# Kernel optimization log

Measured on AMD Instinct MI355X. Metric: run time of the kernel, lower is better.

Reference implementation:

```python
import jax, jax.numpy as jnp
import numpy as np

NUM_HEADS = 16
HEAD_DIM = 64  # embedding_dim 1024 / 16


def setup_inputs() -> dict:
    key = jax.random.key(0)
    k1, k2, k3, k4 = jax.random.split(key, 4)
    B, S, D = 2, 2048, 1024
    return {
        "query": jax.random.normal(k1, (B, S, D), dtype=jnp.float32),
        "key": jax.random.normal(k2, (B, S, D), dtype=jnp.float32),
        "value": jax.random.normal(k3, (B, S, D), dtype=jnp.float32),
        "W_out": jax.random.normal(k4, (D, D), dtype=jnp.float32) * (1.0 / np.sqrt(D)),
        "b_out": jnp.zeros((D,), dtype=jnp.float32),
    }


def reference(query, key, value, W_out, b_out):
    B, S, D = query.shape
    H, hd = NUM_HEADS, HEAD_DIM
    # NOTE: original forward never applies q_fc/k_fc/v_fc (transform ignores fc)
    q = query.reshape(B, S, H, hd).transpose(0, 2, 1, 3)  # [B,H,S,hd]
    k = key.reshape(B, S, H, hd).transpose(0, 2, 1, 3)
    v = value.reshape(B, S, H, hd).transpose(0, 2, 1, 3)
    scores = jnp.einsum("bhqd,bhkd->bhqk", q, k) / jnp.sqrt(jnp.float32(hd))
    probs = jax.nn.softmax(scores, axis=-1)  # mask=None, dropout=None
    ctx = jnp.einsum("bhqk,bhkd->bhqd", probs, v)
    ctx = ctx.transpose(0, 2, 1, 3).reshape(B, S, D)
    return ctx @ W_out.T + b_out
```

## Files before the change

### kernel.cpp

```cpp
#include <hip/hip_runtime.h>
#include <stdint.h>

#define NB 2
#define SEQ 2048
#define DIM 1024
#define NH 16
#define HD 64

typedef __attribute__((ext_vector_type(4))) float f32x4;
typedef __attribute__((ext_vector_type(16))) float f32x16;
typedef __attribute__((ext_vector_type(8))) short s16x8;
typedef __attribute__((ext_vector_type(4))) short s16x4;
typedef __attribute__((ext_vector_type(8))) __bf16 bf16x8;

static __device__ __forceinline__ short f2bf_rne(float x) {
  uint32_t u = __float_as_uint(x);
  u += 0x7fffu + ((u >> 16) & 1u);
  return (short)(u >> 16);
}
static __device__ __forceinline__ float bfbits2f(short h) {
  return __uint_as_float(((uint32_t)(uint16_t)h) << 16);
}
static __device__ __forceinline__ bf16x8 ldfrag(const short* p) {
  bf16x8 r;
  __builtin_memcpy(&r, p, 16);
  return r;
}
static __device__ __forceinline__ void glds16(const short* g, short* l) {
  __builtin_amdgcn_global_load_lds(
      (const __attribute__((address_space(1))) uint32_t*)g,
      (__attribute__((address_space(3))) uint32_t*)l, 16, 0, 0);
}

__global__ __launch_bounds__(256) void prep_kv(const float* __restrict__ K,
                                               const float* __restrict__ V,
                                               short* __restrict__ Kh,
                                               short* __restrict__ Vt) {
  __shared__ float vtile[64][65];
  const int tid = threadIdx.x;
  const int t0 = blockIdx.x * 64;
  const int bh = blockIdx.y;
  const int b = bh >> 4, h = bh & 15;

#pragma unroll
  for (int i = 0; i < 4; ++i) {
    int f = tid + 256 * i;
    int row = f >> 4;
    int col = (f & 15) * 4;
    const float* src = K + ((size_t)(b * SEQ + t0 + row)) * DIM + h * HD + col;
    f32x4 v = *(const f32x4*)src;
    s16x4 hi;
#pragma unroll
    for (int j = 0; j < 4; ++j) hi[j] = f2bf_rne(v[j]);
    *(s16x4*)(Kh + ((size_t)bh * SEQ + t0 + row) * HD + col) = hi;
  }
#pragma unroll
  for (int i = 0; i < 4; ++i) {
    int f = tid + 256 * i;
    int row = f >> 4;
    int col = (f & 15) * 4;
    const float* src = V + ((size_t)(b * SEQ + t0 + row)) * DIM + h * HD + col;
    f32x4 v = *(const f32x4*)src;
#pragma unroll
    for (int j = 0; j < 4; ++j) vtile[row][col + j] = v[j];
  }
  __syncthreads();
#pragma unroll
  for (int i = 0; i < 4; ++i) {
    int idx = tid + 256 * i;
    int d = idx >> 4;
    int kb = (idx & 15) * 4;
    int kp = (kb & ~12) | ((kb & 4) << 1) | ((kb & 8) >> 1);
    s16x4 o4;
#pragma unroll
    for (int j = 0; j < 4; ++j) o4[j] = f2bf_rne(vtile[kb + j][d]);
    *(s16x4*)(Vt + ((size_t)bh * HD + d) * SEQ + t0 + kp) = o4;
  }
}

__global__ __launch_bounds__(256) void prep_w(const float* __restrict__ W,
                                              short* __restrict__ Wh) {
  size_t idx = ((size_t)blockIdx.x * 256 + threadIdx.x) * 8;
  f32x4 a = *(const f32x4*)(W + idx);
  f32x4 b = *(const f32x4*)(W + idx + 4);
  s16x8 o;
#pragma unroll
  for (int j = 0; j < 4; ++j) {
    o[j] = f2bf_rne(a[j]);
    o[4 + j] = f2bf_rne(b[j]);
  }
  *(s16x8*)(Wh + idx) = o;
}

#define QSCALE (0.125f * 1.44269504088896340736f)

__global__ __launch_bounds__(256, 2) void attn(const float* __restrict__ Q,
                                               const short* __restrict__ Kh,
                                               const short* __restrict__ Vt,
                                               short* __restrict__ Ch) {
  __shared__ __align__(16) short ksh[2][64 * 64];
  __shared__ __align__(16) short vts[2][64 * 64];

  const int tid = threadIdx.x;
  const int wv = tid >> 6, ln = tid & 63;
  const int l32 = ln & 31, hl = ln >> 5;
  const int bh = blockIdx.y, b = bh >> 4, hh = bh & 15;
  const int q0 = blockIdx.x * 128 + wv * 32;

  bf16x8 qh[4], ql[4];
  {
    const float* qp = Q + ((size_t)(b * SEQ + q0 + l32)) * DIM + hh * HD + hl * 8;
#pragma unroll
    for (int ks = 0; ks < 4; ++ks) {
      short th[8], tl[8];
#pragma unroll
      for (int j = 0; j < 8; ++j) {
        float x = qp[ks * 16 + j] * QSCALE;
        short hs = f2bf_rne(x);
        th[j] = hs;
        tl[j] = f2bf_rne(x - bfbits2f(hs));
      }
      __builtin_memcpy(&qh[ks], th, 16);
      __builtin_memcpy(&ql[ks], tl, 16);
    }
  }

  f32x16 acc[2];
#pragma unroll
  for (int r = 0; r < 16; ++r) {
    acc[0][r] = 0.f;
    acc[1][r] = 0.f;
  }
  float den = 0.f;

  const short* khg = Kh + (size_t)bh * SEQ * HD;
  const short* vtg = Vt + (size_t)bh * HD * SEQ;

  const int srow8 = ln >> 3;
  const int sg = ln & 7;

#pragma unroll
  for (int i = 0; i < 4; ++i) {
    int c = wv * 4 + i;
    int row = (c & 7) * 8 + srow8;
    int sw = (sg ^ srow8) * 8;
    if (c < 8)
      glds16(khg + (size_t)row * HD + sw, &ksh[0][(c & 7) * 512]);
    else
      glds16(vtg + (size_t)row * SEQ + sw, &vts[0][(c & 7) * 512]);
  }

  for (int t = 0; t < SEQ / 64; ++t) {
    __syncthreads();
    if (t + 1 < SEQ / 64) {
      const int kk = (t + 1) * 64;
      const int bn = (t + 1) & 1;
#pragma unroll
      for (int i = 0; i < 4; ++i) {
        int c = wv * 4 + i;
        int row = (c & 7) * 8 + srow8;
        int sw = (sg ^ srow8) * 8;
        if (c < 8)
          glds16(khg + (size_t)(kk + row) * HD + sw, &ksh[bn][(c & 7) * 512]);
        else
          glds16(vtg + (size_t)row * SEQ + kk + sw, &vts[bn][(c & 7) * 512]);
      }
    }
    const short* kb = ksh[t & 1];
    const short* vbuf = vts[t & 1];

#pragma unroll
    for (int nt = 0; nt < 2; ++nt) {
      f32x16 sf;
#pragma unroll
      for (int r = 0; r < 16; ++r) sf[r] = 0.f;
#pragma unroll
      for (int ks = 0; ks < 4; ++ks) {
        bf16x8 kf =
            ldfrag(kb + (nt * 32 + l32) * 64 + (((ks * 2 + hl) ^ (l32 & 7)) * 8));
        sf = __builtin_amdgcn_mfma_f32_32x32x16_bf16(kf, qh[ks], sf, 0, 0, 0);
        sf = __builtin_amdgcn_mfma_f32_32x32x16_bf16(kf, ql[ks], sf, 0, 0, 0);
      }
#pragma unroll
      for (int tp = 0; tp < 2; ++tp) {
        short pp[8];
#pragma unroll
        for (int j = 0; j < 8; ++j) {
          float p = __builtin_amdgcn_exp2f(sf[tp * 8 + j]);
          den += p;
          uint32_t u = __float_as_uint(p) + 0x8000u;
          pp[j] = (short)(u >> 16);
        }
        bf16x8 pa;
        __builtin_memcpy(&pa, pp, 16);
        const int ksg = nt * 2 + tp;
#pragma unroll
        for (int dt = 0; dt < 2; ++dt) {
          bf16x8 vf = ldfrag(vbuf + (dt * 32 + l32) * 64 +
                             (((ksg * 2 + hl) ^ (l32 & 7)) * 8));
          acc[dt] =
              __builtin_amdgcn_mfma_f32_32x32x16_bf16(pa, vf, acc[dt], 0, 0, 0);
        }
      }
    }
  }

  den += __shfl_xor(den, 32);
  float invd = 1.0f / den;
  float inv_r[16];
#pragma unroll
  for (int r = 0; r < 16; ++r)
    inv_r[r] = __shfl(invd, (r & 3) + 8 * (r >> 2) + 4 * hl, 64);
#pragma unroll
  for (int dt = 0; dt < 2; ++dt)
#pragma unroll
    for (int r = 0; r < 16; ++r) {
      int row = (r & 3) + 8 * (r >> 2) + 4 * hl;
      size_t off = ((size_t)(b * SEQ + q0 + row)) * DIM + hh * HD + dt * 32 + l32;
      Ch[off] = f2bf_rne(acc[dt][r] * inv_r[r]);
    }
}

__global__ __launch_bounds__(256, 2) void proj(const short* __restrict__ Ah,
                                               const short* __restrict__ Wh,
                                               const float* __restrict__ bias,
                                               float* __restrict__ OUT) {
  __shared__ __align__(16) short ash[2][128 * 64];
  __shared__ __align__(16) short wsh[2][64 * 64];
  const int tid = threadIdx.x;
  const int wv = tid >> 6, ln = tid & 63;
  const int l32 = ln & 31, hl = ln >> 5;
  const int m0 = blockIdx.x * 128, n0 = blockIdx.y * 64;

  f32x16 acc[2];
#pragma unroll
  for (int r = 0; r < 16; ++r) {
    acc[0][r] = 0.f;
    acc[1][r] = 0.f;
  }

  const int srow8 = ln >> 3, sg = ln & 7;

#pragma unroll
  for (int i = 0; i < 6; ++i) {
    int c = wv * 6 + i;
    int sw = (sg ^ srow8) * 8;
    if (c < 16) {
      int row = c * 8 + srow8;
      glds16(Ah + (size_t)(m0 + row) * DIM + sw, &ash[0][c * 512]);
    } else {
      int row = (c - 16) * 8 + srow8;
      glds16(Wh + (size_t)(n0 + row) * DIM + sw, &wsh[0][(c - 16) * 512]);
    }
  }

  for (int kt = 0; kt < DIM / 64; ++kt) {
    __syncthreads();
    if (kt + 1 < DIM / 64) {
      const int kk = (kt + 1) * 64;
      const int bn = (kt + 1) & 1;
#pragma unroll
      for (int i = 0; i < 6; ++i) {
        int c = wv * 6 + i;
        int sw = (sg ^ srow8) * 8;
        if (c < 16) {
          int row = c * 8 + srow8;
          glds16(Ah + (size_t)(m0 + row) * DIM + kk + sw, &ash[bn][c * 512]);
        } else {
          int row = (c - 16) * 8 + srow8;
          glds16(Wh + (size_t)(n0 + row) * DIM + kk + sw, &wsh[bn][(c - 16) * 512]);
        }
      }
    }
    const short* ab = ash[kt & 1];
    const short* wb = wsh[kt & 1];
#pragma unroll
    for (int ks = 0; ks < 4; ++ks) {
      bf16x8 af = ldfrag(ab + (wv * 32 + l32) * 64 + (((ks * 2 + hl) ^ (l32 & 7)) * 8));
#pragma unroll
      for (int nt = 0; nt < 2; ++nt) {
        bf16x8 wf =
            ldfrag(wb + (nt * 32 + l32) * 64 + (((ks * 2 + hl) ^ (l32 & 7)) * 8));
        acc[nt] = __builtin_amdgcn_mfma_f32_32x32x16_bf16(af, wf, acc[nt], 0, 0, 0);
      }
    }
  }

  float bs[2];
#pragma unroll
  for (int nt = 0; nt < 2; ++nt) bs[nt] = bias[n0 + nt * 32 + l32];
#pragma unroll
  for (int nt = 0; nt < 2; ++nt)
#pragma unroll
    for (int r = 0; r < 16; ++r) {
      int row = m0 + wv * 32 + (r & 3) + 8 * (r >> 2) + 4 * hl;
      int col = n0 + nt * 32 + l32;
      OUT[(size_t)row * DIM + col] = acc[nt][r] + bs[nt];
    }
}

extern "C" void kernel_launch(void* const* d_in, const int* in_sizes, int n_in,
                              void* d_out, int out_size, void* d_ws, size_t ws_size,
                              hipStream_t stream) {
  const float* Q = (const float*)d_in[0];
  const float* K = (const float*)d_in[1];
  const float* V = (const float*)d_in[2];
  const float* W = (const float*)d_in[3];
  const float* bias = (const float*)d_in[4];
  float* OUT = (float*)d_out;

  char* ws = (char*)d_ws;
  short* Kh = (short*)(ws + ((size_t)0 << 20));
  short* Vt = (short*)(ws + ((size_t)8 << 20));
  short* Ch = (short*)(ws + ((size_t)16 << 20));
  short* Wh = (short*)(ws + ((size_t)24 << 20));

  prep_kv<<<dim3(SEQ / 64, NB * NH), 256, 0, stream>>>(K, V, Kh, Vt);
  prep_w<<<dim3((DIM * DIM) / 2048), 256, 0, stream>>>(W, Wh);
  attn<<<dim3(SEQ / 128, NB * NH), 256, 0, stream>>>(Q, Kh, Vt, Ch);
  proj<<<dim3((NB * SEQ) / 128, DIM / 64), 256, 0, stream>>>(Ch, Wh, bias, OUT);
}
```

Before: 171.5 us.

## Drop split-bf16 Q correction, pack exp probs with bf16x2, merge prep kernels

Removes the low-order bf16 residual of Q, which halves the QK^T MFMA count in the attention kernel but lowers score precision to plain bf16. The softmax numerator is now packed with a paired float-to-bf16x2 round-to-nearest conversion and two separate denominator accumulators. The K/V and W prep kernels are merged into one launch with 1536 blocks to save one kernel launch. The main cost targeted is the doubled MFMA work in the score computation; the tradeoff is reduced accuracy.

```diff
diff --git a/kernel.cpp b/kernel.cpp
--- a/kernel.cpp
+++ b/kernel.cpp
@@ -1,4 +1,5 @@
 #include <hip/hip_runtime.h>
+#include <hip/hip_bf16.h>
 #include <stdint.h>
 
 #define NB 2
@@ -18,8 +19,11 @@
   u += 0x7fffu + ((u >> 16) & 1u);
   return (short)(u >> 16);
 }
-static __device__ __forceinline__ float bfbits2f(short h) {
-  return __uint_as_float(((uint32_t)(uint16_t)h) << 16);
+static __device__ __forceinline__ uint32_t pk_bf16(float a, float b) {
+  __hip_bfloat162 h = __float22bfloat162_rn(float2{a, b});
+  uint32_t u;
+  __builtin_memcpy(&u, &h, 4);
+  return u;
 }
 static __device__ __forceinline__ bf16x8 ldfrag(const short* p) {
   bf16x8 r;
@@ -32,14 +36,32 @@
       (__attribute__((address_space(3))) uint32_t*)l, 16, 0, 0);
 }
 
-__global__ __launch_bounds__(256) void prep_kv(const float* __restrict__ K,
-                                               const float* __restrict__ V,
-                                               short* __restrict__ Kh,
-                                               short* __restrict__ Vt) {
+__global__ __launch_bounds__(256) void prep_all(const float* __restrict__ K,
+                                                const float* __restrict__ V,
+                                                const float* __restrict__ W,
+                                                short* __restrict__ Kh,
+                                                short* __restrict__ Vt,
+                                                short* __restrict__ Wh) {
   __shared__ float vtile[64][65];
   const int tid = threadIdx.x;
-  const int t0 = blockIdx.x * 64;
-  const int bh = blockIdx.y;
+  const int id = blockIdx.x;
+
+  if (id >= 1024) {
+    size_t idx = ((size_t)(id - 1024) * 256 + tid) * 8;
+    f32x4 a = *(const f32x4*)(W + idx);
+    f32x4 b = *(const f32x4*)(W + idx + 4);
+    s16x8 o;
+#pragma unroll
+    for (int j = 0; j < 4; ++j) {
+      o[j] = f2bf_rne(a[j]);
+      o[4 + j] = f2bf_rne(b[j]);
+    }
+    *(s16x8*)(Wh + idx) = o;
+    return;
+  }
+
+  const int t0 = (id & 31) * 64;
+  const int bh = id >> 5;
   const int b = bh >> 4, h = bh & 15;
 
 #pragma unroll
@@ -78,20 +100,6 @@
   }
 }
 
-__global__ __launch_bounds__(256) void prep_w(const float* __restrict__ W,
-                                              short* __restrict__ Wh) {
-  size_t idx = ((size_t)blockIdx.x * 256 + threadIdx.x) * 8;
-  f32x4 a = *(const f32x4*)(W + idx);
-  f32x4 b = *(const f32x4*)(W + idx + 4);
-  s16x8 o;
-#pragma unroll
-  for (int j = 0; j < 4; ++j) {
-    o[j] = f2bf_rne(a[j]);
-    o[4 + j] = f2bf_rne(b[j]);
-  }
-  *(s16x8*)(Wh + idx) = o;
-}
-
 #define QSCALE (0.125f * 1.44269504088896340736f)
 
 __global__ __launch_bounds__(256, 2) void attn(const float* __restrict__ Q,
@@ -107,21 +115,15 @@
   const int bh = blockIdx.y, b = bh >> 4, hh = bh & 15;
   const int q0 = blockIdx.x * 128 + wv * 32;
 
-  bf16x8 qh[4], ql[4];
+  bf16x8 qh[4];
   {
     const float* qp = Q + ((size_t)(b * SEQ + q0 + l32)) * DIM + hh * HD + hl * 8;
 #pragma unroll
     for (int ks = 0; ks < 4; ++ks) {
-      short th[8], tl[8];
-#pragma unroll
-      for (int j = 0; j < 8; ++j) {
-        float x = qp[ks * 16 + j] * QSCALE;
-        short hs = f2bf_rne(x);
-        th[j] = hs;
-        tl[j] = f2bf_rne(x - bfbits2f(hs));
-      }
+      short th[8];
+#pragma unroll
+      for (int j = 0; j < 8; ++j) th[j] = f2bf_rne(qp[ks * 16 + j] * QSCALE);
       __builtin_memcpy(&qh[ks], th, 16);
-      __builtin_memcpy(&ql[ks], tl, 16);
     }
   }
 
@@ -131,7 +133,7 @@
     acc[0][r] = 0.f;
     acc[1][r] = 0.f;
   }
-  float den = 0.f;
+  float den0 = 0.f, den1 = 0.f;
 
   const short* khg = Kh + (size_t)bh * SEQ * HD;
   const short* vtg = Vt + (size_t)bh * HD * SEQ;
@@ -179,20 +181,20 @@
         bf16x8 kf =
             ldfrag(kb + (nt * 32 + l32) * 64 + (((ks * 2 + hl) ^ (l32 & 7)) * 8));
         sf = __builtin_amdgcn_mfma_f32_32x32x16_bf16(kf, qh[ks], sf, 0, 0, 0);
-        sf = __builtin_amdgcn_mfma_f32_32x32x16_bf16(kf, ql[ks], sf, 0, 0, 0);
       }
 #pragma unroll
       for (int tp = 0; tp < 2; ++tp) {
-        short pp[8];
-#pragma unroll
-        for (int j = 0; j < 8; ++j) {
-          float p = __builtin_amdgcn_exp2f(sf[tp * 8 + j]);
-          den += p;
-          uint32_t u = __float_as_uint(p) + 0x8000u;
-          pp[j] = (short)(u >> 16);
+        uint32_t w[4];
+#pragma unroll
+        for (int j2 = 0; j2 < 4; ++j2) {
+          float p0 = __builtin_amdgcn_exp2f(sf[tp * 8 + j2 * 2]);
+          float p1 = __builtin_amdgcn_exp2f(sf[tp * 8 + j2 * 2 + 1]);
+          den0 += p0;
+          den1 += p1;
+          w[j2] = pk_bf16(p0, p1);
         }
         bf16x8 pa;
-        __builtin_memcpy(&pa, pp, 16);
+        __builtin_memcpy(&pa, w, 16);
         const int ksg = nt * 2 + tp;
 #pragma unroll
         for (int dt = 0; dt < 2; ++dt) {
@@ -205,6 +207,7 @@
     }
   }
 
+  float den = den0 + den1;
   den += __shfl_xor(den, 32);
   float invd = 1.0f / den;
   float inv_r[16];
@@ -315,8 +318,7 @@
   short* Ch = (short*)(ws + ((size_t)16 << 20));
   short* Wh = (short*)(ws + ((size_t)24 << 20));
 
-  prep_kv<<<dim3(SEQ / 64, NB * NH), 256, 0, stream>>>(K, V, Kh, Vt);
-  prep_w<<<dim3((DIM * DIM) / 2048), 256, 0, stream>>>(W, Wh);
+  prep_all<<<dim3(1536), 256, 0, stream>>>(K, V, W, Kh, Vt, Wh);
   attn<<<dim3(SEQ / 128, NB * NH), 256, 0, stream>>>(Q, Kh, Vt, Ch);
   proj<<<dim3((NB * SEQ) / 128, DIM / 64), 256, 0, stream>>>(Ch, Wh, bias, OUT);
 }
```

Measured after the change: 162.9 us. 5.0% less time.
